# Optimization experiments

Hardware: AMD Instinct MI355X
Metric: run time of the kernel (lower is better)

The kernel has to match this reference:

```python
import jax, jax.numpy as jnp
import numpy as np

S_NUM, E_NUM, K, B = 50000, 20000, 128, 8192
N = S_NUM + E_NUM
N_EDGES = 1000000
LAYERS = 3


def setup_inputs() -> dict:
    key = jax.random.key(0)
    ks = jax.random.split(key, 16)
    return {
        "stu_emb": jax.random.normal(ks[0], (S_NUM, K), jnp.float32),
        "exer_emb": jax.random.normal(ks[1], (E_NUM, K), jnp.float32),
        "kn_emb": jax.random.normal(ks[2], (K, K), jnp.float32),
        "disc_emb": jax.random.normal(ks[3], (E_NUM, 1), jnp.float32),
        "right_W": jax.random.normal(ks[4], (LAYERS, K, K), jnp.float32) * (1.0 / np.sqrt(K)),
        "wrong_W": jax.random.normal(ks[5], (LAYERS, K, K), jnp.float32) * (1.0 / np.sqrt(K)),
        "right_ci": jax.random.uniform(ks[6], (N, 1), jnp.float32),
        "right_cj": jax.random.uniform(ks[7], (N, 1), jnp.float32),
        "wrong_ci": jax.random.uniform(ks[8], (N, 1), jnp.float32),
        "wrong_cj": jax.random.uniform(ks[9], (N, 1), jnp.float32),
        "right_edges": jax.random.randint(ks[10], (2, N_EDGES), 0, N, jnp.int64),
        "wrong_edges": jax.random.randint(ks[11], (2, N_EDGES), 0, N, jnp.int64),
        "student_id": jax.random.randint(ks[12], (B,), 0, S_NUM, jnp.int64),
        "exercise_id": jax.random.randint(ks[13], (B,), 0, E_NUM, jnp.int64),
    }


def _gcmc_layer(feat, W, cj, ci, src, dst, n_nodes):
    # dense projection + src-side normalizer (dropout is identity in eval)
    h = (feat @ W) * cj                    # [N, K]
    # copy_u/sum message passing: scatter-add messages to destination nodes
    agg = jax.ops.segment_sum(h[src], dst, num_segments=n_nodes)  # [N, K]
    return agg * ci


def _graph_forward(feat, Ws, ci, cj, edges, n_nodes):
    src, dst = edges[0], edges[1]
    for i in range(Ws.shape[0]):
        feat = _gcmc_layer(feat, Ws[i], cj, ci, src, dst, n_nodes)
    return feat


def reference(stu_emb, exer_emb, kn_emb, disc_emb, right_W, wrong_W,
              right_ci, right_cj, wrong_ci, wrong_cj,
              right_edges, wrong_edges, student_id, exercise_id):
    n_students = stu_emb.shape[0]
    n_nodes = stu_emb.shape[0] + exer_emb.shape[0]
    all_weight = jnp.concatenate([stu_emb, exer_emb], axis=0)  # [N, K]
    w1 = _graph_forward(all_weight, right_W, right_ci, right_cj, right_edges, n_nodes)
    w2 = _graph_forward(all_weight, wrong_W, wrong_ci, wrong_cj, wrong_edges, n_nodes)
    stu_forward = w1[:n_students] + w2[:n_students]
    exer_forward = w1[n_students:] + w2[n_students:]
    batch_stu_ts = stu_forward[student_id]      # [B, K]
    batch_exer_ts = exer_forward[exercise_id]   # [B, K]
    disc_ts = disc_emb[exercise_id]             # [B, 1]
    knowledge_ts = kn_emb                       # [K, K]
    return (batch_stu_ts, batch_exer_ts, disc_ts, knowledge_ts)
```

## Files before the change

kernel.cpp:

```cpp
#include <hip/hip_runtime.h>
#include <hip/hip_bf16.h>
#include <stdint.h>

#define S_NUM 50000
#define E_NUM 20000
#define NNODE 70000
#define KDIM 128
#define BATCH 8192
#define NEDGE 1000000

#define NRANGE 128
#define RSZ 547
#define BUCKET_CAP 8448
#define CHUNK 8192
#define BINCAP 120
#define GR 256

typedef __attribute__((ext_vector_type(8))) short short8;
typedef __attribute__((ext_vector_type(4))) float f32x4;

__device__ __forceinline__ float bf2f(ushort u) {
    union { uint32_t i; float f; } v; v.i = ((uint32_t)u) << 16; return v.f;
}
__device__ __forceinline__ ushort f2bf(float f) {
    union { uint32_t i; float f; } v; v.f = f;
    uint32_t r = v.i + 0x7fffu + ((v.i >> 16) & 1u);
    return (ushort)(r >> 16);
}
__device__ __forceinline__ float hi2f(uint32_t u) {
    union { uint32_t i; float f; } v; v.i = u & 0xffff0000u; return v.f;
}
__device__ __forceinline__ float lo2f(uint32_t u) {
    union { uint32_t i; float f; } v; v.i = u << 16; return v.f;
}

__global__ void zero_k(int* __restrict__ p, int n) {
    for (int i = blockIdx.x * blockDim.x + threadIdx.x; i < n; i += gridDim.x * blockDim.x)
        p[i] = 0;
}

__global__ void prepW_k(const float* __restrict__ rW, const float* __restrict__ wW,
                        ushort* __restrict__ ws) {
    int i = blockIdx.x * blockDim.x + threadIdx.x;
    if (i >= 6 * 16384) return;
    int m = i >> 14, idx = i & 16383;
    const float* W = (m < 3) ? rW + m * 16384 : wW + (m - 3) * 16384;
    float x = W[idx];
    int k = idx >> 7, c = idx & 127;
    ushort hb = f2bf(x);
    ushort lb = f2bf(x - bf2f(hb));
    int off = ((c * 256 + 2 * k) ^ ((c & 7) << 4)) >> 1;
    ws[(size_t)m * 32768 + off] = hb;
    ws[(size_t)m * 32768 + 16384 + off] = lb;
}

__global__ __launch_bounds__(256) void bucket_k(const int* __restrict__ redge,
                                                const int* __restrict__ wedge,
                                                int* __restrict__ gbcnt,
                                                uint32_t* __restrict__ bpk) {
    __shared__ uint32_t lpk[NRANGE][BINCAP];
    __shared__ int lcnt[NRANGE];
    __shared__ int gbase[NRANGE];
    const int NB = (NEDGE + CHUNK - 1) / CHUNK;
    int bid = blockIdx.x;
    int graph = bid >= NB;
    int cb = graph ? bid - NB : bid;
    const int* eg = graph ? wedge : redge;
    int e0 = cb * CHUNK;
    int nthis = min(CHUNK, NEDGE - e0);
    for (int i = threadIdx.x; i < NRANGE; i += 256) lcnt[i] = 0;
    __syncthreads();
    for (int i = threadIdx.x; i < nthis; i += 256) {
        int s = eg[e0 + i];
        int d = eg[NEDGE + e0 + i];
        int b = d / RSZ;
        uint32_t p = ((uint32_t)(d - b * RSZ) << 17) | (uint32_t)s;
        int slot = atomicAdd(&lcnt[b], 1);
        if (slot < BINCAP) lpk[b][slot] = p;
        else {
            int gs = atomicAdd(&gbcnt[graph * NRANGE + b], 1);
            if (gs < BUCKET_CAP)
                bpk[(size_t)(graph * NRANGE + b) * BUCKET_CAP + gs] = p;
        }
    }
    __syncthreads();
    for (int b = threadIdx.x; b < NRANGE; b += 256) {
        int c = min(lcnt[b], BINCAP);
        lcnt[b] = c;
        gbase[b] = atomicAdd(&gbcnt[graph * NRANGE + b], c);
    }
    __syncthreads();
    for (int b = 0; b < NRANGE; ++b) {
        int c = lcnt[b];
        size_t base = (size_t)(graph * NRANGE + b) * BUCKET_CAP + gbase[b];
        for (int i = threadIdx.x; i < c; i += 256)
            if (gbase[b] + i < BUCKET_CAP) bpk[base + i] = lpk[b][i];
    }
}

__global__ __launch_bounds__(256) void build_k(const uint32_t* __restrict__ bpk,
                                               const int* __restrict__ gbcnt,
                                               int* __restrict__ rp,
                                               int* __restrict__ csr) {
    __shared__ int lcnt[RSZ + 1];
    __shared__ int lexcl[RSZ];
    __shared__ int lcur[RSZ];
    __shared__ int sliceA[BUCKET_CAP];
    __shared__ int sliceB[BUCKET_CAP];
    __shared__ int tcur[64];
    __shared__ int wsum[4];
    __shared__ int s_base, s_carry;
    int combo = blockIdx.x;
    int graph = combo >> 7, grp = combo & (NRANGE - 1);
    int lo = grp * RSZ;
    int rsize = min(RSZ, NNODE - lo);
    int n = min(gbcnt[combo], BUCKET_CAP);
    const uint32_t* bp = bpk + (size_t)combo * BUCKET_CAP;
    int* rpg = rp + graph * (NNODE + 1);
    int* og = csr + graph * NEDGE;
    int tid = threadIdx.x, lane = tid & 63, wid = tid >> 6;

    if (tid < NRANGE) lcnt[tid] = min(gbcnt[graph * NRANGE + tid], BUCKET_CAP);
    if (tid < 64) tcur[tid] = 0;
    __syncthreads();
    if (tid == 0) {
        int b = 0;
        for (int i = 0; i < grp; ++i) b += lcnt[i];
        s_base = b;
        s_carry = 0;
    }
    __syncthreads();
    for (int i = tid; i < n; i += 256)
        atomicAdd(&tcur[(bp[i] & 0x1FFFFu) >> 12], 1);
    __syncthreads();
    if (wid == 0) {
        int v = (lane < 18) ? tcur[lane] : 0;
        int incl = v;
        #pragma unroll
        for (int off = 1; off < 32; off <<= 1) {
            int t = __shfl_up(incl, off, 64);
            if (lane >= off) incl += t;
        }
        if (lane < 18) tcur[lane] = incl - v;
    }
    __syncthreads();
    for (int i = tid; i < n; i += 256) {
        uint32_t p = bp[i];
        int t = (p & 0x1FFFFu) >> 12;
        sliceA[atomicAdd(&tcur[t], 1)] = (int)p;
    }
    __syncthreads();
    for (int i = tid; i < rsize; i += 256) lcnt[i] = 0;
    __syncthreads();
    for (int i = tid; i < n; i += 256)
        atomicAdd(&lcnt[((uint32_t)sliceA[i]) >> 17], 1);
    __syncthreads();
    for (int base = 0; base < rsize; base += 256) {
        int i = base + tid;
        int v = (i < rsize) ? lcnt[i] : 0;
        int incl = v;
        #pragma unroll
        for (int off = 1; off < 64; off <<= 1) {
            int t = __shfl_up(incl, off, 64);
            if (lane >= off) incl += t;
        }
        if (lane == 63) wsum[wid] = incl;
        __syncthreads();
        int carry = s_carry;
        if (wid == 0 && lane < 4) {
            int wv = wsum[lane];
            #pragma unroll
            for (int off = 1; off < 4; off <<= 1) {
                int t = __shfl_up(wv, off, 64);
                if (lane >= off) wv += t;
            }
            wsum[lane] = wv;
        }
        __syncthreads();
        int waveoff = (wid == 0) ? 0 : wsum[wid - 1];
        int excl = carry + waveoff + incl - v;
        if (i < rsize) { lexcl[i] = excl; lcur[i] = excl; }
        __syncthreads();
        if (tid == 0) s_carry = carry + wsum[3];
        __syncthreads();
    }
    int gbas = s_base;
    for (int i = tid; i < rsize; i += 256)
        rpg[lo + i] = gbas + lexcl[i];
    if (grp == NRANGE - 1 && tid == 0) rpg[NNODE] = gbas + n;
    for (int i = tid; i < n; i += 256) {
        uint32_t p = (uint32_t)sliceA[i];
        int slot = atomicAdd(&lcur[p >> 17], 1);
        sliceB[slot] = (int)(p & 0x1FFFFu);
    }
    __syncthreads();
    for (int i = tid; i < n; i += 256)
        og[gbas + i] = sliceB[i];
}

__global__ __launch_bounds__(256) void cvt1_k(const float* __restrict__ stu,
                                              const float* __restrict__ exer,
                                              uint4* __restrict__ featb) {
    const int total = NNODE * 16;
    for (int i = blockIdx.x * blockDim.x + threadIdx.x; i < total;
         i += gridDim.x * blockDim.x) {
        int node = i >> 4;
        int qq = i & 15;
        const float4* src = (const float4*)((node < S_NUM)
                              ? stu + (size_t)node * KDIM
                              : exer + (size_t)(node - S_NUM) * KDIM);
        float4 a = src[qq * 2];
        float4 b = src[qq * 2 + 1];
        uint4 o;
        o.x = (uint32_t)f2bf(a.x) | ((uint32_t)f2bf(a.y) << 16);
        o.y = (uint32_t)f2bf(a.z) | ((uint32_t)f2bf(a.w) << 16);
        o.z = (uint32_t)f2bf(b.x) | ((uint32_t)f2bf(b.y) << 16);
        o.w = (uint32_t)f2bf(b.z) | ((uint32_t)f2bf(b.w) << 16);
        featb[i] = o;
    }
}

__global__ __launch_bounds__(256) void agg2_k(const uint4* __restrict__ fcR,
                                              const uint4* __restrict__ fcW,
                                              const float* __restrict__ cjR,
                                              const float* __restrict__ cjW,
                                              const int* __restrict__ rp,
                                              const int* __restrict__ csr,
                                              uint4* __restrict__ outR,
                                              uint4* __restrict__ outW,
                                              int useCj) {
    int gn = (blockIdx.x * blockDim.x + threadIdx.x) >> 6;
    if (gn >= 2 * NNODE) return;
    int graph = gn >= NNODE;
    int n = graph ? gn - NNODE : gn;
    const uint4* fc = graph ? fcW : fcR;
    const float* cjg = graph ? cjW : cjR;
    const int* rpg = rp + graph * (NNODE + 1);
    const int* cs = csr + graph * NEDGE;
    uint4* outp = graph ? outW : outR;

    int lane = threadIdx.x & 63;
    int rowgrp = lane >> 4, c16 = lane & 15;
    int beg = rpg[n], end = rpg[n + 1];
    float acc[8];
    #pragma unroll
    for (int j = 0; j < 8; ++j) acc[j] = 0.f;

    if (useCj) {
        for (int e = beg; e < end; e += 8) {
            int r0 = e + rowgrp, r1 = e + 4 + rowgrp;
            int s0 = (r0 < end) ? cs[r0] : -1;
            int s1 = (r1 < end) ? cs[r1] : -1;
            uint4 u0 = {0, 0, 0, 0}, u1 = {0, 0, 0, 0};
            float c0 = 0.f, c1 = 0.f;
            if (s0 >= 0) { u0 = fc[(size_t)s0 * 16 + c16]; c0 = cjg[s0]; }
            if (s1 >= 0) { u1 = fc[(size_t)s1 * 16 + c16]; c1 = cjg[s1]; }
            acc[0] = fmaf(c0, lo2f(u0.x), fmaf(c1, lo2f(u1.x), acc[0]));
            acc[1] = fmaf(c0, hi2f(u0.x), fmaf(c1, hi2f(u1.x), acc[1]));
            acc[2] = fmaf(c0, lo2f(u0.y), fmaf(c1, lo2f(u1.y), acc[2]));
            acc[3] = fmaf(c0, hi2f(u0.y), fmaf(c1, hi2f(u1.y), acc[3]));
            acc[4] = fmaf(c0, lo2f(u0.z), fmaf(c1, lo2f(u1.z), acc[4]));
            acc[5] = fmaf(c0, hi2f(u0.z), fmaf(c1, hi2f(u1.z), acc[5]));
            acc[6] = fmaf(c0, lo2f(u0.w), fmaf(c1, lo2f(u1.w), acc[6]));
            acc[7] = fmaf(c0, hi2f(u0.w), fmaf(c1, hi2f(u1.w), acc[7]));
        }
    } else {
        for (int e = beg; e < end; e += 8) {
            int r0 = e + rowgrp, r1 = e + 4 + rowgrp;
            uint4 u0 = {0, 0, 0, 0}, u1 = {0, 0, 0, 0};
            if (r0 < end) u0 = fc[(size_t)cs[r0] * 16 + c16];
            if (r1 < end) u1 = fc[(size_t)cs[r1] * 16 + c16];
            acc[0] += lo2f(u0.x) + lo2f(u1.x);
            acc[1] += hi2f(u0.x) + hi2f(u1.x);
            acc[2] += lo2f(u0.y) + lo2f(u1.y);
            acc[3] += hi2f(u0.y) + hi2f(u1.y);
            acc[4] += lo2f(u0.z) + lo2f(u1.z);
            acc[5] += hi2f(u0.z) + hi2f(u1.z);
            acc[6] += lo2f(u0.w) + lo2f(u1.w);
            acc[7] += hi2f(u0.w) + hi2f(u1.w);
        }
    }
    #pragma unroll
    for (int j = 0; j < 8; ++j) {
        acc[j] += __shfl_xor(acc[j], 16, 64);
        acc[j] += __shfl_xor(acc[j], 32, 64);
    }
    if (rowgrp == 0) {
        uint4 o;
        o.x = (uint32_t)f2bf(acc[0]) | ((uint32_t)f2bf(acc[1]) << 16);
        o.y = (uint32_t)f2bf(acc[2]) | ((uint32_t)f2bf(acc[3]) << 16);
        o.z = (uint32_t)f2bf(acc[4]) | ((uint32_t)f2bf(acc[5]) << 16);
        o.w = (uint32_t)f2bf(acc[6]) | ((uint32_t)f2bf(acc[7]) << 16);
        outp[(size_t)n * 16 + c16] = o;
    }
}

__global__ __launch_bounds__(256) void gemm2_k(const ushort* __restrict__ AR,
                                               const ushort* __restrict__ AW,
                                               const ushort* __restrict__ wsR,
                                               const ushort* __restrict__ wsW,
                                               const float* __restrict__ rci,
                                               const float* __restrict__ rcj,
                                               const float* __restrict__ wci,
                                               const float* __restrict__ wcj,
                                               ushort* __restrict__ outR,
                                               ushort* __restrict__ outW,
                                               int mode) {
    const int halfBlocks = (NNODE + GR - 1) / GR;
    int graph = blockIdx.x >= halfBlocks;
    int bb = graph ? blockIdx.x - halfBlocks : blockIdx.x;
    const ushort* A = graph ? AW : AR;
    const ushort* wsm = graph ? wsW : wsR;
    const float* ci = graph ? wci : rci;
    const float* cj = graph ? wcj : rcj;
    ushort* outB = graph ? outW : outR;

    __shared__ ushort wt[32768];
    {
        const uint4* g = (const uint4*)wsm;
        uint4* l = (uint4*)wt;
        for (int i = threadIdx.x; i < 4096; i += 256) l[i] = g[i];
    }
    __syncthreads();

    int wid = threadIdx.x >> 6, lane = threadIdx.x & 63;
    int q = lane >> 4, l16 = lane & 15;
    int rbase = bb * GR + wid * 64;

    short8 z8 = {0, 0, 0, 0, 0, 0, 0, 0};
    short8 afr[4][4];
    #pragma unroll
    for (int t = 0; t < 4; ++t) {
        int row = rbase + t * 16 + l16;
        bool rok = row < NNODE;
        const short8* ar = (const short8*)(A + (size_t)row * KDIM);
        #pragma unroll
        for (int kb = 0; kb < 4; ++kb)
            afr[t][kb] = rok ? ar[kb * 4 + q] : z8;
    }
    float scal[4][4];
    #pragma unroll
    for (int t = 0; t < 4; ++t)
        #pragma unroll
        for (int b = 0; b < 4; ++b) {
            int r = rbase + t * 16 + q * 4 + b;
            scal[t][b] = (r < NNODE) ? (mode ? ci[r] * cj[r] : ci[r]) : 0.f;
        }

    #pragma unroll
    for (int cb = 0; cb < 8; ++cb) {
        int c = cb * 16 + l16;
        short8 bHi[4], bLo[4];
        #pragma unroll
        for (int kb = 0; kb < 4; ++kb) {
            int byte = (c * 256 + 2 * (kb * 32 + q * 8)) ^ ((c & 7) << 4);
            bHi[kb] = *(const short8*)((const char*)wt + byte);
            bLo[kb] = *(const short8*)((const char*)wt + 32768 + byte);
        }
        #pragma unroll
        for (int t = 0; t < 4; ++t) {
            f32x4 acc = {0.f, 0.f, 0.f, 0.f};
            #pragma unroll
            for (int kb = 0; kb < 4; ++kb) {
                acc = __builtin_amdgcn_mfma_f32_16x16x32_bf16(afr[t][kb], bHi[kb], acc, 0, 0, 0);
                acc = __builtin_amdgcn_mfma_f32_16x16x32_bf16(afr[t][kb], bLo[kb], acc, 0, 0, 0);
            }
            #pragma unroll
            for (int b = 0; b < 4; ++b) {
                int r = rbase + t * 16 + q * 4 + b;
                if (r < NNODE)
                    outB[(size_t)r * KDIM + c] = f2bf(acc[b] * scal[t][b]);
            }
        }
    }
}

__global__ void out_k(const ushort* __restrict__ w1, const ushort* __restrict__ w2,
                      const float* __restrict__ disc, const float* __restrict__ kn,
                      const int* __restrict__ sid, const int* __restrict__ eid,
                      float* __restrict__ out) {
    const int total = 2 * BATCH * KDIM + BATCH + KDIM * KDIM;
    for (int i = blockIdx.x * blockDim.x + threadIdx.x; i < total;
         i += gridDim.x * blockDim.x) {
        if (i < BATCH * KDIM) {
            int b = i >> 7, c = i & 127;
            size_t n = (size_t)sid[b];
            out[i] = bf2f(w1[n * KDIM + c]) + bf2f(w2[n * KDIM + c]);
        } else if (i < 2 * BATCH * KDIM) {
            int j = i - BATCH * KDIM;
            int b = j >> 7, c = j & 127;
            size_t n = (size_t)(S_NUM + eid[b]);
            out[i] = bf2f(w1[n * KDIM + c]) + bf2f(w2[n * KDIM + c]);
        } else if (i < 2 * BATCH * KDIM + BATCH) {
            out[i] = disc[eid[i - 2 * BATCH * KDIM]];
        } else {
            out[i] = kn[i - (2 * BATCH * KDIM + BATCH)];
        }
    }
}

static inline size_t align_up(size_t x) { return (x + 255) & ~(size_t)255; }

extern "C" void kernel_launch(void* const* d_in, const int* in_sizes, int n_in,
                              void* d_out, int out_size, void* d_ws, size_t ws_size,
                              hipStream_t stream) {
    const float* stu  = (const float*)d_in[0];
    const float* exer = (const float*)d_in[1];
    const float* kn   = (const float*)d_in[2];
    const float* disc = (const float*)d_in[3];
    const float* rW   = (const float*)d_in[4];
    const float* wW   = (const float*)d_in[5];
    const float* rci  = (const float*)d_in[6];
    const float* rcj  = (const float*)d_in[7];
    const float* wci  = (const float*)d_in[8];
    const float* wcj  = (const float*)d_in[9];
    const int* redge   = (const int*)d_in[10];
    const int* wedge   = (const int*)d_in[11];
    const int* sid     = (const int*)d_in[12];
    const int* eid     = (const int*)d_in[13];
    float* out         = (float*)d_out;

    char* p = (char*)d_ws;
    const size_t fB16 = align_up((size_t)NNODE * KDIM * 2);
    ushort* featb = (ushort*)p; p += fB16;
    ushort* fcR = (ushort*)p; p += fB16;
    ushort* fcW = (ushort*)p; p += fB16;
    ushort* pR  = (ushort*)p; p += fB16;
    ushort* pW  = (ushort*)p; p += fB16;
    ushort* ws  = (ushort*)p; p += align_up((size_t)6 * 32768 * 2);
    int* gbcnt = (int*)p; p += align_up((size_t)256 * 4);
    int* rp  = (int*)p; p += align_up((size_t)2 * (NNODE + 1) * 4);
    int* csr = (int*)p; p += align_up((size_t)2 * NEDGE * 4);
    uint32_t* bpk = (uint32_t*)pR;

    const int gemmBlocks2 = 2 * ((NNODE + GR - 1) / GR);
    const int aggBlocks2 = (2 * NNODE * 64) / 256;
    const int NB = (NEDGE + CHUNK - 1) / CHUNK;

    prepW_k<<<(6 * 16384 + 255) / 256, 256, 0, stream>>>(rW, wW, ws);
    zero_k<<<1, 256, 0, stream>>>(gbcnt, 256);
    bucket_k<<<2 * NB, 256, 0, stream>>>(redge, wedge, gbcnt, bpk);
    build_k<<<256, 256, 0, stream>>>(bpk, gbcnt, rp, csr);
    cvt1_k<<<2048, 256, 0, stream>>>(stu, exer, (uint4*)featb);

    agg2_k<<<aggBlocks2, 256, 0, stream>>>((const uint4*)featb, (const uint4*)featb,
                                           rcj, wcj, rp, csr, (uint4*)pR, (uint4*)pW, 1);
    gemm2_k<<<gemmBlocks2, 256, 0, stream>>>(pR, pW, ws + 0 * 32768, ws + 3 * 32768,
                                             rci, rcj, wci, wcj, fcR, fcW, 1);
    agg2_k<<<aggBlocks2, 256, 0, stream>>>((const uint4*)fcR, (const uint4*)fcW,
                                           nullptr, nullptr, rp, csr, (uint4*)pR, (uint4*)pW, 0);
    gemm2_k<<<gemmBlocks2, 256, 0, stream>>>(pR, pW, ws + 1 * 32768, ws + 4 * 32768,
                                             rci, rcj, wci, wcj, fcR, fcW, 1);
    agg2_k<<<aggBlocks2, 256, 0, stream>>>((const uint4*)fcR, (const uint4*)fcW,
                                           nullptr, nullptr, rp, csr, (uint4*)pR, (uint4*)pW, 0);
    gemm2_k<<<gemmBlocks2, 256, 0, stream>>>(pR, pW, ws + 2 * 32768, ws + 5 * 32768,
                                             rci, rcj, wci, wcj, fcR, fcW, 0);

    out_k<<<2048, 256, 0, stream>>>(fcR, fcW, disc, kn, sid, eid, out);
}
```

Measured before the change: 414.5 us.

## Pad CSR rows to multiples of 16 with sentinel node to drop bounds checks

The CSR build now places each range bucket at a fixed stride and pads every destination row's edge list up to a multiple of 16 with a sentinel node index. That sentinel points at a zeroed extra feature row and a zero cj entry. The aggregation kernel can then walk edges 16 at a time with four unconditional gathers per lane and packed two-wide float math, with no per-edge bounds checks or masking. It also removes the tile sort pass in build_k and folds the counter zeroing into prepW_k. In exchange, padding adds wasted gathers for low-degree rows and needs begin/end pointer arrays plus a larger CSR buffer.

```diff
diff --git a/kernel.cpp b/kernel.cpp
--- a/kernel.cpp
+++ b/kernel.cpp
@@ -12,12 +12,14 @@
 #define NRANGE 128
 #define RSZ 547
 #define BUCKET_CAP 8448
+#define RCAP 16672
 #define CHUNK 8192
 #define BINCAP 120
 #define GR 256
 
 typedef __attribute__((ext_vector_type(8))) short short8;
 typedef __attribute__((ext_vector_type(4))) float f32x4;
+typedef __attribute__((ext_vector_type(2))) float f32x2;
 
 __device__ __forceinline__ float bf2f(ushort u) {
     union { uint32_t i; float f; } v; v.i = ((uint32_t)u) << 16; return v.f;
@@ -27,20 +29,15 @@
     uint32_t r = v.i + 0x7fffu + ((v.i >> 16) & 1u);
     return (ushort)(r >> 16);
 }
-__device__ __forceinline__ float hi2f(uint32_t u) {
-    union { uint32_t i; float f; } v; v.i = u & 0xffff0000u; return v.f;
-}
-__device__ __forceinline__ float lo2f(uint32_t u) {
-    union { uint32_t i; float f; } v; v.i = u << 16; return v.f;
-}
-
-__global__ void zero_k(int* __restrict__ p, int n) {
-    for (int i = blockIdx.x * blockDim.x + threadIdx.x; i < n; i += gridDim.x * blockDim.x)
-        p[i] = 0;
+__device__ __forceinline__ f32x2 up2(uint32_t u) {
+    union { uint32_t i; float f; } lo, hi;
+    lo.i = u << 16; hi.i = u & 0xffff0000u;
+    f32x2 r; r.x = lo.f; r.y = hi.f; return r;
 }
 
 __global__ void prepW_k(const float* __restrict__ rW, const float* __restrict__ wW,
-                        ushort* __restrict__ ws) {
+                        ushort* __restrict__ ws, int* __restrict__ gbcnt) {
+    if (blockIdx.x == 0 && threadIdx.x < 256) gbcnt[threadIdx.x] = 0;
     int i = blockIdx.x * blockDim.x + threadIdx.x;
     if (i >= 6 * 16384) return;
     int m = i >> 14, idx = i & 16383;
@@ -100,60 +97,33 @@
 
 __global__ __launch_bounds__(256) void build_k(const uint32_t* __restrict__ bpk,
                                                const int* __restrict__ gbcnt,
-                                               int* __restrict__ rp,
+                                               int* __restrict__ rpb,
+                                               int* __restrict__ rpe,
                                                int* __restrict__ csr) {
-    __shared__ int lcnt[RSZ + 1];
+    __shared__ int lcnt[RSZ];
     __shared__ int lexcl[RSZ];
+    __shared__ int pexcl[RSZ];
     __shared__ int lcur[RSZ];
-    __shared__ int sliceA[BUCKET_CAP];
     __shared__ int sliceB[BUCKET_CAP];
-    __shared__ int tcur[64];
     __shared__ int wsum[4];
-    __shared__ int s_base, s_carry;
+    __shared__ int s_carry;
     int combo = blockIdx.x;
     int graph = combo >> 7, grp = combo & (NRANGE - 1);
     int lo = grp * RSZ;
     int rsize = min(RSZ, NNODE - lo);
     int n = min(gbcnt[combo], BUCKET_CAP);
     const uint32_t* bp = bpk + (size_t)combo * BUCKET_CAP;
-    int* rpg = rp + graph * (NNODE + 1);
-    int* og = csr + graph * NEDGE;
+    int* rpbg = rpb + graph * NNODE;
+    int* rpeg = rpe + graph * NNODE;
+    int* og = csr + (size_t)combo * RCAP;
+    const int rbase = combo * RCAP;
     int tid = threadIdx.x, lane = tid & 63, wid = tid >> 6;
 
-    if (tid < NRANGE) lcnt[tid] = min(gbcnt[graph * NRANGE + tid], BUCKET_CAP);
-    if (tid < 64) tcur[tid] = 0;
-    __syncthreads();
-    if (tid == 0) {
-        int b = 0;
-        for (int i = 0; i < grp; ++i) b += lcnt[i];
-        s_base = b;
-        s_carry = 0;
-    }
+    for (int i = tid; i < rsize; i += 256) lcnt[i] = 0;
+    if (tid == 0) s_carry = 0;
     __syncthreads();
     for (int i = tid; i < n; i += 256)
-        atomicAdd(&tcur[(bp[i] & 0x1FFFFu) >> 12], 1);
-    __syncthreads();
-    if (wid == 0) {
-        int v = (lane < 18) ? tcur[lane] : 0;
-        int incl = v;
-        #pragma unroll
-        for (int off = 1; off < 32; off <<= 1) {
-            int t = __shfl_up(incl, off, 64);
-            if (lane >= off) incl += t;
-        }
-        if (lane < 18) tcur[lane] = incl - v;
-    }
-    __syncthreads();
-    for (int i = tid; i < n; i += 256) {
-        uint32_t p = bp[i];
-        int t = (p & 0x1FFFFu) >> 12;
-        sliceA[atomicAdd(&tcur[t], 1)] = (int)p;
-    }
-    __syncthreads();
-    for (int i = tid; i < rsize; i += 256) lcnt[i] = 0;
-    __syncthreads();
-    for (int i = tid; i < n; i += 256)
-        atomicAdd(&lcnt[((uint32_t)sliceA[i]) >> 17], 1);
+        atomicAdd(&lcnt[bp[i] >> 17], 1);
     __syncthreads();
     for (int base = 0; base < rsize; base += 256) {
         int i = base + tid;
@@ -184,39 +154,100 @@
         if (tid == 0) s_carry = carry + wsum[3];
         __syncthreads();
     }
-    int gbas = s_base;
-    for (int i = tid; i < rsize; i += 256)
-        rpg[lo + i] = gbas + lexcl[i];
-    if (grp == NRANGE - 1 && tid == 0) rpg[NNODE] = gbas + n;
+    if (tid == 0) s_carry = 0;
+    __syncthreads();
+    for (int base = 0; base < rsize; base += 256) {
+        int i = base + tid;
+        int v = (i < rsize) ? ((lcnt[i] + 15) & ~15) : 0;
+        int incl = v;
+        #pragma unroll
+        for (int off = 1; off < 64; off <<= 1) {
+            int t = __shfl_up(incl, off, 64);
+            if (lane >= off) incl += t;
+        }
+        if (lane == 63) wsum[wid] = incl;
+        __syncthreads();
+        int carry = s_carry;
+        if (wid == 0 && lane < 4) {
+            int wv = wsum[lane];
+            #pragma unroll
+            for (int off = 1; off < 4; off <<= 1) {
+                int t = __shfl_up(wv, off, 64);
+                if (lane >= off) wv += t;
+            }
+            wsum[lane] = wv;
+        }
+        __syncthreads();
+        int waveoff = (wid == 0) ? 0 : wsum[wid - 1];
+        int excl = carry + waveoff + incl - v;
+        if (i < rsize) pexcl[i] = excl;
+        __syncthreads();
+        if (tid == 0) s_carry = carry + wsum[3];
+        __syncthreads();
+    }
+    for (int i = tid; i < rsize; i += 256) {
+        int pc = (lcnt[i] + 15) & ~15;
+        rpbg[lo + i] = rbase + pexcl[i];
+        rpeg[lo + i] = rbase + pexcl[i] + pc;
+    }
     for (int i = tid; i < n; i += 256) {
-        uint32_t p = (uint32_t)sliceA[i];
+        uint32_t p = bp[i];
         int slot = atomicAdd(&lcur[p >> 17], 1);
-        sliceB[slot] = (int)(p & 0x1FFFFu);
-    }
-    __syncthreads();
-    for (int i = tid; i < n; i += 256)
-        og[gbas + i] = sliceB[i];
+        sliceB[slot] = (int)p;
+    }
+    __syncthreads();
+    for (int i = tid; i < n; i += 256) {
+        uint32_t p = (uint32_t)sliceB[i];
+        int r = p >> 17;
+        og[pexcl[r] + (i - lexcl[r])] = (int)(p & 0x1FFFFu);
+    }
+    for (int r = tid; r < rsize; r += 256) {
+        int c = lcnt[r], pc = (c + 15) & ~15, b = pexcl[r];
+        for (int j = c; j < pc; ++j) og[b + j] = NNODE;
+    }
 }
 
 __global__ __launch_bounds__(256) void cvt1_k(const float* __restrict__ stu,
                                               const float* __restrict__ exer,
-                                              uint4* __restrict__ featb) {
-    const int total = NNODE * 16;
+                                              const float* __restrict__ rcj,
+                                              const float* __restrict__ wcj,
+                                              uint4* __restrict__ featb,
+                                              uint4* __restrict__ fcR,
+                                              uint4* __restrict__ fcW,
+                                              float* __restrict__ cjpR,
+                                              float* __restrict__ cjpW) {
+    const int main = NNODE * 16;
+    const int total = main + 48 + 2 * (NNODE + 1);
+    const uint4 z4 = {0, 0, 0, 0};
     for (int i = blockIdx.x * blockDim.x + threadIdx.x; i < total;
          i += gridDim.x * blockDim.x) {
-        int node = i >> 4;
-        int qq = i & 15;
-        const float4* src = (const float4*)((node < S_NUM)
-                              ? stu + (size_t)node * KDIM
-                              : exer + (size_t)(node - S_NUM) * KDIM);
-        float4 a = src[qq * 2];
-        float4 b = src[qq * 2 + 1];
-        uint4 o;
-        o.x = (uint32_t)f2bf(a.x) | ((uint32_t)f2bf(a.y) << 16);
-        o.y = (uint32_t)f2bf(a.z) | ((uint32_t)f2bf(a.w) << 16);
-        o.z = (uint32_t)f2bf(b.x) | ((uint32_t)f2bf(b.y) << 16);
-        o.w = (uint32_t)f2bf(b.z) | ((uint32_t)f2bf(b.w) << 16);
-        featb[i] = o;
+        if (i < main) {
+            int node = i >> 4;
+            int qq = i & 15;
+            const float4* src = (const float4*)((node < S_NUM)
+                                  ? stu + (size_t)node * KDIM
+                                  : exer + (size_t)(node - S_NUM) * KDIM);
+            float4 a = src[qq * 2];
+            float4 b = src[qq * 2 + 1];
+            uint4 o;
+            o.x = (uint32_t)f2bf(a.x) | ((uint32_t)f2bf(a.y) << 16);
+            o.y = (uint32_t)f2bf(a.z) | ((uint32_t)f2bf(a.w) << 16);
+            o.z = (uint32_t)f2bf(b.x) | ((uint32_t)f2bf(b.y) << 16);
+            o.w = (uint32_t)f2bf(b.z) | ((uint32_t)f2bf(b.w) << 16);
+            featb[i] = o;
+        } else if (i < main + 48) {
+            int j = i - main;
+            if (j < 16)      featb[(size_t)NNODE * 16 + j] = z4;
+            else if (j < 32) fcR[(size_t)NNODE * 16 + (j - 16)] = z4;
+            else             fcW[(size_t)NNODE * 16 + (j - 32)] = z4;
+        } else {
+            int k = i - main - 48;
+            if (k <= NNODE)  cjpR[k] = (k < NNODE) ? rcj[k] : 0.f;
+            else {
+                int m = k - (NNODE + 1);
+                cjpW[m] = (m < NNODE) ? wcj[m] : 0.f;
+            }
+        }
     }
 }
 
@@ -224,7 +255,8 @@
                                               const uint4* __restrict__ fcW,
                                               const float* __restrict__ cjR,
                                               const float* __restrict__ cjW,
-                                              const int* __restrict__ rp,
+                                              const int* __restrict__ rpb,
+                                              const int* __restrict__ rpe,
                                               const int* __restrict__ csr,
                                               uint4* __restrict__ outR,
                                               uint4* __restrict__ outW,
@@ -235,62 +267,60 @@
     int n = graph ? gn - NNODE : gn;
     const uint4* fc = graph ? fcW : fcR;
     const float* cjg = graph ? cjW : cjR;
-    const int* rpg = rp + graph * (NNODE + 1);
-    const int* cs = csr + graph * NEDGE;
+    const int* rpbg = rpb + graph * NNODE;
+    const int* rpeg = rpe + graph * NNODE;
     uint4* outp = graph ? outW : outR;
 
     int lane = threadIdx.x & 63;
     int rowgrp = lane >> 4, c16 = lane & 15;
-    int beg = rpg[n], end = rpg[n + 1];
-    float acc[8];
-    #pragma unroll
-    for (int j = 0; j < 8; ++j) acc[j] = 0.f;
+    int beg = rpbg[n], end = rpeg[n];
+    f32x2 acc0 = {0.f, 0.f}, acc1 = {0.f, 0.f}, acc2v = {0.f, 0.f}, acc3 = {0.f, 0.f};
 
     if (useCj) {
-        for (int e = beg; e < end; e += 8) {
-            int r0 = e + rowgrp, r1 = e + 4 + rowgrp;
-            int s0 = (r0 < end) ? cs[r0] : -1;
-            int s1 = (r1 < end) ? cs[r1] : -1;
-            uint4 u0 = {0, 0, 0, 0}, u1 = {0, 0, 0, 0};
-            float c0 = 0.f, c1 = 0.f;
-            if (s0 >= 0) { u0 = fc[(size_t)s0 * 16 + c16]; c0 = cjg[s0]; }
-            if (s1 >= 0) { u1 = fc[(size_t)s1 * 16 + c16]; c1 = cjg[s1]; }
-            acc[0] = fmaf(c0, lo2f(u0.x), fmaf(c1, lo2f(u1.x), acc[0]));
-            acc[1] = fmaf(c0, hi2f(u0.x), fmaf(c1, hi2f(u1.x), acc[1]));
-            acc[2] = fmaf(c0, lo2f(u0.y), fmaf(c1, lo2f(u1.y), acc[2]));
-            acc[3] = fmaf(c0, hi2f(u0.y), fmaf(c1, hi2f(u1.y), acc[3]));
-            acc[4] = fmaf(c0, lo2f(u0.z), fmaf(c1, lo2f(u1.z), acc[4]));
-            acc[5] = fmaf(c0, hi2f(u0.z), fmaf(c1, hi2f(u1.z), acc[5]));
-            acc[6] = fmaf(c0, lo2f(u0.w), fmaf(c1, lo2f(u1.w), acc[6]));
-            acc[7] = fmaf(c0, hi2f(u0.w), fmaf(c1, hi2f(u1.w), acc[7]));
+        for (int e = beg; e < end; e += 16) {
+            int s0 = csr[e + rowgrp];
+            int s1 = csr[e + 4 + rowgrp];
+            int s2 = csr[e + 8 + rowgrp];
+            int s3 = csr[e + 12 + rowgrp];
+            uint4 u0 = fc[(size_t)s0 * 16 + c16];
+            uint4 u1 = fc[(size_t)s1 * 16 + c16];
+            uint4 u2 = fc[(size_t)s2 * 16 + c16];
+            uint4 u3 = fc[(size_t)s3 * 16 + c16];
+            float c0 = cjg[s0], c1 = cjg[s1], c2 = cjg[s2], c3 = cjg[s3];
+            f32x2 v0 = {c0, c0}, v1 = {c1, c1}, v2 = {c2, c2}, v3 = {c3, c3};
+            acc0 += v0 * up2(u0.x) + v1 * up2(u1.x) + v2 * up2(u2.x) + v3 * up2(u3.x);
+            acc1 += v0 * up2(u0.y) + v1 * up2(u1.y) + v2 * up2(u2.y) + v3 * up2(u3.y);
+            acc2v += v0 * up2(u0.z) + v1 * up2(u1.z) + v2 * up2(u2.z) + v3 * up2(u3.z);
+            acc3 += v0 * up2(u0.w) + v1 * up2(u1.w) + v2 * up2(u2.w) + v3 * up2(u3.w);
         }
     } else {
-        for (int e = beg; e < end; e += 8) {
-            int r0 = e + rowgrp, r1 = e + 4 + rowgrp;
-            uint4 u0 = {0, 0, 0, 0}, u1 = {0, 0, 0, 0};
-            if (r0 < end) u0 = fc[(size_t)cs[r0] * 16 + c16];
-            if (r1 < end) u1 = fc[(size_t)cs[r1] * 16 + c16];
-            acc[0] += lo2f(u0.x) + lo2f(u1.x);
-            acc[1] += hi2f(u0.x) + hi2f(u1.x);
-            acc[2] += lo2f(u0.y) + lo2f(u1.y);
-            acc[3] += hi2f(u0.y) + hi2f(u1.y);
-            acc[4] += lo2f(u0.z) + lo2f(u1.z);
-            acc[5] += hi2f(u0.z) + hi2f(u1.z);
-            acc[6] += lo2f(u0.w) + lo2f(u1.w);
-            acc[7] += hi2f(u0.w) + hi2f(u1.w);
-        }
-    }
+        for (int e = beg; e < end; e += 16) {
+            int s0 = csr[e + rowgrp];
+            int s1 = csr[e + 4 + rowgrp];
+            int s2 = csr[e + 8 + rowgrp];
+            int s3 = csr[e + 12 + rowgrp];
+            uint4 u0 = fc[(size_t)s0 * 16 + c16];
+            uint4 u1 = fc[(size_t)s1 * 16 + c16];
+            uint4 u2 = fc[(size_t)s2 * 16 + c16];
+            uint4 u3 = fc[(size_t)s3 * 16 + c16];
+            acc0 += (up2(u0.x) + up2(u1.x)) + (up2(u2.x) + up2(u3.x));
+            acc1 += (up2(u0.y) + up2(u1.y)) + (up2(u2.y) + up2(u3.y));
+            acc2v += (up2(u0.z) + up2(u1.z)) + (up2(u2.z) + up2(u3.z));
+            acc3 += (up2(u0.w) + up2(u1.w)) + (up2(u2.w) + up2(u3.w));
+        }
+    }
+    float a[8] = {acc0.x, acc0.y, acc1.x, acc1.y, acc2v.x, acc2v.y, acc3.x, acc3.y};
     #pragma unroll
     for (int j = 0; j < 8; ++j) {
-        acc[j] += __shfl_xor(acc[j], 16, 64);
-        acc[j] += __shfl_xor(acc[j], 32, 64);
+        a[j] += __shfl_xor(a[j], 16, 64);
+        a[j] += __shfl_xor(a[j], 32, 64);
     }
     if (rowgrp == 0) {
         uint4 o;
-        o.x = (uint32_t)f2bf(acc[0]) | ((uint32_t)f2bf(acc[1]) << 16);
-        o.y = (uint32_t)f2bf(acc[2]) | ((uint32_t)f2bf(acc[3]) << 16);
-        o.z = (uint32_t)f2bf(acc[4]) | ((uint32_t)f2bf(acc[5]) << 16);
-        o.w = (uint32_t)f2bf(acc[6]) | ((uint32_t)f2bf(acc[7]) << 16);
+        o.x = (uint32_t)f2bf(a[0]) | ((uint32_t)f2bf(a[1]) << 16);
+        o.y = (uint32_t)f2bf(a[2]) | ((uint32_t)f2bf(a[3]) << 16);
+        o.z = (uint32_t)f2bf(a[4]) | ((uint32_t)f2bf(a[5]) << 16);
+        o.w = (uint32_t)f2bf(a[6]) | ((uint32_t)f2bf(a[7]) << 16);
         outp[(size_t)n * 16 + c16] = o;
     }
 }
@@ -421,7 +451,7 @@
     float* out         = (float*)d_out;
 
     char* p = (char*)d_ws;
-    const size_t fB16 = align_up((size_t)NNODE * KDIM * 2);
+    const size_t fB16 = align_up((size_t)(NNODE + 1) * KDIM * 2);
     ushort* featb = (ushort*)p; p += fB16;
     ushort* fcR = (ushort*)p; p += fB16;
     ushort* fcW = (ushort*)p; p += fB16;
@@ -429,30 +459,36 @@
     ushort* pW  = (ushort*)p; p += fB16;
     ushort* ws  = (ushort*)p; p += align_up((size_t)6 * 32768 * 2);
     int* gbcnt = (int*)p; p += align_up((size_t)256 * 4);
-    int* rp  = (int*)p; p += align_up((size_t)2 * (NNODE + 1) * 4);
-    int* csr = (int*)p; p += align_up((size_t)2 * NEDGE * 4);
+    int* rpb = (int*)p; p += align_up((size_t)2 * NNODE * 4);
+    int* rpe = (int*)p; p += align_up((size_t)2 * NNODE * 4);
+    int* csr = (int*)p; p += align_up((size_t)256 * RCAP * 4);
+    float* cjpR = (float*)p; p += align_up((size_t)(NNODE + 1) * 4);
+    float* cjpW = (float*)p; p += align_up((size_t)(NNODE + 1) * 4);
     uint32_t* bpk = (uint32_t*)pR;
 
     const int gemmBlocks2 = 2 * ((NNODE + GR - 1) / GR);
     const int aggBlocks2 = (2 * NNODE * 64) / 256;
     const int NB = (NEDGE + CHUNK - 1) / CHUNK;
 
-    prepW_k<<<(6 * 16384 + 255) / 256, 256, 0, stream>>>(rW, wW, ws);
-    zero_k<<<1, 256, 0, stream>>>(gbcnt, 256);
+    prepW_k<<<(6 * 16384 + 255) / 256, 256, 0, stream>>>(rW, wW, ws, gbcnt);
     bucket_k<<<2 * NB, 256, 0, stream>>>(redge, wedge, gbcnt, bpk);
-    build_k<<<256, 256, 0, stream>>>(bpk, gbcnt, rp, csr);
-    cvt1_k<<<2048, 256, 0, stream>>>(stu, exer, (uint4*)featb);
+    build_k<<<256, 256, 0, stream>>>(bpk, gbcnt, rpb, rpe, csr);
+    cvt1_k<<<2048, 256, 0, stream>>>(stu, exer, rcj, wcj, (uint4*)featb,
+                                     (uint4*)fcR, (uint4*)fcW, cjpR, cjpW);
 
     agg2_k<<<aggBlocks2, 256, 0, stream>>>((const uint4*)featb, (const uint4*)featb,
-                                           rcj, wcj, rp, csr, (uint4*)pR, (uint4*)pW, 1);
+                                           cjpR, cjpW, rpb, rpe, csr,
+                                           (uint4*)pR, (uint4*)pW, 1);
     gemm2_k<<<gemmBlocks2, 256, 0, stream>>>(pR, pW, ws + 0 * 32768, ws + 3 * 32768,
                                              rci, rcj, wci, wcj, fcR, fcW, 1);
     agg2_k<<<aggBlocks2, 256, 0, stream>>>((const uint4*)fcR, (const uint4*)fcW,
-                                           nullptr, nullptr, rp, csr, (uint4*)pR, (uint4*)pW, 0);
+                                           nullptr, nullptr, rpb, rpe, csr,
+                                           (uint4*)pR, (uint4*)pW, 0);
     gemm2_k<<<gemmBlocks2, 256, 0, stream>>>(pR, pW, ws + 1 * 32768, ws + 4 * 32768,
                                              rci, rcj, wci, wcj, fcR, fcW, 1);
     agg2_k<<<aggBlocks2, 256, 0, stream>>>((const uint4*)fcR, (const uint4*)fcW,
-                                           nullptr, nullptr, rp, csr, (uint4*)pR, (uint4*)pW, 0);
+                                           nullptr, nullptr, rpb, rpe, csr,
+                                           (uint4*)pR, (uint4*)pW, 0);
     gemm2_k<<<gemmBlocks2, 256, 0, stream>>>(pR, pW, ws + 2 * 32768, ws + 5 * 32768,
                                              rci, rcj, wci, wcj, fcR, fcW, 0);
 
```

New measurement: 393.7 us. 1.05x faster.
